# Performance work log

Hardware: AMD Instinct MI355X
Metric: run time of the kernel (lower is better)

Reference implementation:

```python
import jax, jax.numpy as jnp
import numpy as np

EMBED_DIM = 1024
NUM_HEADS = 16
HEAD_DIM = EMBED_DIM // NUM_HEADS
LN_EPS = 1e-5


def setup_inputs() -> dict:
    key = jax.random.key(0)
    ks = jax.random.split(key, 7)
    B, N, D = 4, 2048, EMBED_DIM
    s = 1.0 / np.sqrt(D)  # ~kaiming-uniform scale for Linear weights
    return {
        "inputs": jax.random.normal(ks[0], (B, N, D), dtype=jnp.float32),
        "W_q": jax.random.uniform(ks[1], (D, D), jnp.float32, -s, s),
        "W_k": jax.random.uniform(ks[2], (D, D), jnp.float32, -s, s),
        "W_v": jax.random.uniform(ks[3], (D, D), jnp.float32, -s, s),
        "W_o": jax.random.uniform(ks[4], (D, D), jnp.float32, -s, s),
        "ln_gamma": jnp.ones((D,), jnp.float32),
        "ln_beta": jnp.zeros((D,), jnp.float32),
    }


def reference(inputs, W_q, W_k, W_v, W_o, ln_gamma, ln_beta):
    x = inputs
    B, N, D = x.shape
    H, Hd = NUM_HEADS, HEAD_DIM
    # torch nn.Linear computes x @ W.T; W_* stored as (out, in)
    q = (x @ W_q.T).reshape(B, N, H, Hd).transpose(0, 2, 1, 3)  # [B,H,N,Hd]
    k = (x @ W_k.T).reshape(B, N, H, Hd).transpose(0, 2, 1, 3)
    v = (x @ W_v.T).reshape(B, N, H, Hd).transpose(0, 2, 1, 3)
    scores = jnp.einsum("bhqd,bhkd->bhqk", q, k) / jnp.sqrt(jnp.float32(Hd))
    attn = jax.nn.softmax(scores, axis=-1)  # dropout p=0 -> identity
    out = jnp.einsum("bhqk,bhkd->bhqd", attn, v)
    out = out.transpose(0, 2, 1, 3).reshape(B, N, D)
    out = out @ W_o.T
    # residual + LayerNorm
    y = out + x
    mu = jnp.mean(y, axis=-1, keepdims=True)
    var = jnp.mean(jnp.square(y - mu), axis=-1, keepdims=True)
    y = (y - mu) * jax.lax.rsqrt(var + LN_EPS)
    return y * ln_gamma + ln_beta
```

## Files before the change

### kernel.cpp

```cpp
#include <hip/hip_runtime.h>
#include <hip/hip_bf16.h>
#include <stdint.h>

typedef __attribute__((ext_vector_type(8))) short bf16x8;
typedef __attribute__((ext_vector_type(4))) float f32x4;

#define GLOBAL_AS __attribute__((address_space(1)))
#define LDS_AS    __attribute__((address_space(3)))

__device__ __forceinline__ void load_lds16(const void* g, void* l) {
  __builtin_amdgcn_global_load_lds((const GLOBAL_AS void*)g, (LDS_AS void*)l, 16, 0, 0);
}

__device__ __forceinline__ short f2bfn(float f) {
  __hip_bfloat16 h = __float2bfloat16(f);
  return __builtin_bit_cast(short, h);
}
__device__ __forceinline__ float bf2f(short s) {
  return __uint_as_float(((unsigned)(unsigned short)s) << 16);
}

__global__ __launch_bounds__(256) void cvt_all(const float* __restrict__ x,
                                               const float* __restrict__ q,
                                               const float* __restrict__ k,
                                               const float* __restrict__ v,
                                               const float* __restrict__ o,
                                               short* __restrict__ xb,
                                               short* __restrict__ Wb,
                                               short* __restrict__ Wob) {
  const int bid = blockIdx.x;
  const float* src;
  short* dst;
  int i;
  if (bid < 4096) {
    src = x; dst = xb; i = (bid * 256 + threadIdx.x) * 8;
  } else {
    const int sel = (bid - 4096) >> 9;
    const int inner = (bid - 4096) & 511;
    i = (inner * 256 + threadIdx.x) * 8;
    src = sel == 0 ? q : sel == 1 ? k : sel == 2 ? v : o;
    dst = sel == 0 ? Wb : sel == 1 ? Wb + 1024 * 1024
        : sel == 2 ? Wb + 2 * 1024 * 1024 : Wob;
  }
  float4 a = *(const float4*)(src + i);
  float4 b = *(const float4*)(src + i + 4);
  bf16x8 ov;
  ov[0] = f2bfn(a.x); ov[1] = f2bfn(a.y); ov[2] = f2bfn(a.z); ov[3] = f2bfn(a.w);
  ov[4] = f2bfn(b.x); ov[5] = f2bfn(b.y); ov[6] = f2bfn(b.z); ov[7] = f2bfn(b.w);
  *(bf16x8*)(dst + i) = ov;
}

__global__ __launch_bounds__(256) void gemm_qkvt(const short* __restrict__ xb,
                                                 const short* __restrict__ Wqk,
                                                 const short* __restrict__ Wv,
                                                 short* __restrict__ qkv,
                                                 short* __restrict__ VT) {
  __shared__ short As[128 * 64];
  __shared__ short Bs[128 * 64];
  const int t = threadIdx.x, l = t & 63, w = t >> 6;
  const int g = l >> 4, li = l & 15;
  const int wr = w >> 1, wc = w & 1;
  const int bid = blockIdx.x;
  const bool isqk = bid < 1024;
  const short* A;
  const short* B;
  int bm, bn;
  if (isqk) {
    A = xb; B = Wqk;
    bm = (bid & 7) * 8 + ((bid >> 3) & 7);
    bn = bid >> 6;
  } else {
    const int b2 = bid - 1024;
    A = Wv; B = xb;
    bm = b2 & 7;
    bn = b2 >> 3;
  }
  const int sw = li & 7;
  const int K = 1024;
  f32x4 acc[4][4] = {};
  const size_t arow0 = (size_t)(bm * 128) * K;
  const size_t brow0 = (size_t)(bn * 128) * K;
  for (int k0 = 0; k0 < K; k0 += 64) {
    __syncthreads();
#pragma unroll
    for (int it = 0; it < 4; ++it) {
      int e = it * 2048 + t * 8;
      int r = e >> 6;
      int cs = (e >> 3) & 7;
      int cg = cs ^ (r & 7);
      load_lds16(A + arow0 + (size_t)r * K + (k0 + cg * 8), &As[e]);
      load_lds16(B + brow0 + (size_t)r * K + (k0 + cg * 8), &Bs[e]);
    }
    __syncthreads();
#pragma unroll
    for (int kk = 0; kk < 2; ++kk) {
      bf16x8 af[4], bfr[4];
#pragma unroll
      for (int m = 0; m < 4; ++m)
        af[m] = *(const bf16x8*)&As[(wr * 64 + m * 16 + li) * 64 + (((kk * 4 + g) ^ sw) * 8)];
#pragma unroll
      for (int n = 0; n < 4; ++n)
        bfr[n] = *(const bf16x8*)&Bs[(wc * 64 + n * 16 + li) * 64 + (((kk * 4 + g) ^ sw) * 8)];
#pragma unroll
      for (int m = 0; m < 4; ++m)
#pragma unroll
        for (int n = 0; n < 4; ++n)
          acc[m][n] = __builtin_amdgcn_mfma_f32_16x16x32_bf16(af[m], bfr[n], acc[m][n], 0, 0, 0);
    }
  }
#pragma unroll
  for (int m = 0; m < 4; ++m)
#pragma unroll
    for (int n = 0; n < 4; ++n)
#pragma unroll
      for (int r = 0; r < 4; ++r) {
        int row = bm * 128 + wr * 64 + m * 16 + g * 4 + r;
        int col = bn * 128 + wc * 64 + n * 16 + li;
        if (isqk)
          qkv[(size_t)row * 3072 + col] = f2bfn(acc[m][n][r]);
        else
          VT[(size_t)(col >> 11) * (1024 * 2048) + (size_t)row * 2048 +
             (col & 2047)] = f2bfn(acc[m][n][r]);
      }
}

__global__ __launch_bounds__(256) void gemm_projres(const short* __restrict__ A,
                                                    const short* __restrict__ B,
                                                    const float* __restrict__ x,
                                                    short* __restrict__ Up) {
  __shared__ short As[128 * 64];
  __shared__ short Bs[128 * 64];
  const int t = threadIdx.x, l = t & 63, w = t >> 6;
  const int g = l >> 4, li = l & 15;
  const int wr = w >> 1, wc = w & 1;
  const int bid = blockIdx.x;
  const int bm = (bid & 7) * 8 + ((bid >> 3) & 7);
  const int bn = bid >> 6;
  const int sw = li & 7;
  const int K = 1024;
  f32x4 acc[4][4] = {};
  const size_t arow0 = (size_t)(bm * 128) * K;
  const size_t brow0 = (size_t)(bn * 128) * K;
  for (int k0 = 0; k0 < K; k0 += 64) {
    __syncthreads();
#pragma unroll
    for (int it = 0; it < 4; ++it) {
      int e = it * 2048 + t * 8;
      int r = e >> 6;
      int cs = (e >> 3) & 7;
      int cg = cs ^ (r & 7);
      load_lds16(A + arow0 + (size_t)r * K + (k0 + cg * 8), &As[e]);
      load_lds16(B + brow0 + (size_t)r * K + (k0 + cg * 8), &Bs[e]);
    }
    __syncthreads();
#pragma unroll
    for (int kk = 0; kk < 2; ++kk) {
      bf16x8 af[4], bfr[4];
#pragma unroll
      for (int m = 0; m < 4; ++m)
        af[m] = *(const bf16x8*)&As[(wr * 64 + m * 16 + li) * 64 + (((kk * 4 + g) ^ sw) * 8)];
#pragma unroll
      for (int n = 0; n < 4; ++n)
        bfr[n] = *(const bf16x8*)&Bs[(wc * 64 + n * 16 + li) * 64 + (((kk * 4 + g) ^ sw) * 8)];
#pragma unroll
      for (int m = 0; m < 4; ++m)
#pragma unroll
        for (int n = 0; n < 4; ++n)
          acc[m][n] = __builtin_amdgcn_mfma_f32_16x16x32_bf16(af[m], bfr[n], acc[m][n], 0, 0, 0);
    }
  }
#pragma unroll
  for (int m = 0; m < 4; ++m)
#pragma unroll
    for (int n = 0; n < 4; ++n)
#pragma unroll
      for (int r = 0; r < 4; ++r) {
        int row = bm * 128 + wr * 64 + m * 16 + g * 4 + r;
        int col = bn * 128 + wc * 64 + n * 16 + li;
        float v = acc[m][n][r] + x[(size_t)row * 1024 + col];
        Up[(size_t)row * 1024 + col] = f2bfn(v);
      }
}

__global__ __launch_bounds__(512, 4) void attn_fwd(const short* __restrict__ qkv,
                                                   const short* __restrict__ VT,
                                                   short* __restrict__ obuf) {
  const int f0 = blockIdx.x;
  const int work = (f0 & 7) * 64 + (f0 >> 3);
  const int qt = work & 7;
  const int bh = work >> 3;
  const int b = bh >> 4, h = bh & 15;
  const int t = threadIdx.x, w = t >> 6, l = t & 63;
  const int g = l >> 4, li = l & 15;

  __shared__ short Ks[2][64 * 64];
  __shared__ short Vts[2][64 * 64];
  __shared__ short Ps[8][2][16 * 64];

  const size_t base = (size_t)b * 2048 * 3072 + (size_t)h * 64;
  const short* Vsrc = VT + (size_t)bh * 64 * 2048;

  bf16x8 qf[2][2];
  {
    const float QSC = 0.125f * 1.44269504088896341f;
#pragma unroll
    for (int qh = 0; qh < 2; ++qh) {
      const short* qp = qkv + base + (size_t)(qt * 256 + w * 32 + qh * 16 + li) * 3072;
#pragma unroll
      for (int c = 0; c < 2; ++c) {
        bf16x8 v = *(const bf16x8*)(qp + c * 32 + g * 8);
#pragma unroll
        for (int i = 0; i < 8; ++i) {
          float f = bf2f(v[i]);
          v[i] = f2bfn(f * QSC);
        }
        qf[qh][c] = v;
      }
    }
  }

  bf16x8 ones;
#pragma unroll
  for (int i = 0; i < 8; ++i) ones[i] = (short)0x3F80;

  f32x4 o_[2][4], lacc[2];
#pragma unroll
  for (int qh = 0; qh < 2; ++qh) {
#pragma unroll
    for (int dj = 0; dj < 4; ++dj) o_[qh][dj] = (f32x4){0.f, 0.f, 0.f, 0.f};
    lacc[qh] = (f32x4){0.f, 0.f, 0.f, 0.f};
  }

  const int sw = li & 7;

#define STAGE(buf, kt_)                                                          \
  {                                                                              \
    int e = t * 8;                                                               \
    int r = e >> 6;                                                              \
    int cs = (e >> 3) & 7;                                                       \
    int cg = cs ^ (r & 7);                                                       \
    load_lds16(qkv + base + 1024 + (size_t)((kt_) * 64 + r) * 3072 + cg * 8,     \
               &Ks[buf][e]);                                                     \
    load_lds16(Vsrc + (size_t)r * 2048 + (kt_) * 64 + cg * 8, &Vts[buf][e]);     \
  }

  STAGE(0, 0);
  asm volatile("s_waitcnt vmcnt(0)" ::: "memory");
  __syncthreads();

  for (int kt = 0; kt < 32; ++kt) {
    const int cur = kt & 1;
    if (kt + 1 < 32) STAGE(cur ^ 1, kt + 1);

    f32x4 s_[2][4];
#pragma unroll
    for (int qh = 0; qh < 2; ++qh)
#pragma unroll
      for (int j = 0; j < 4; ++j) s_[qh][j] = (f32x4){0.f, 0.f, 0.f, 0.f};
    __builtin_amdgcn_s_setprio(1);
#pragma unroll
    for (int c = 0; c < 2; ++c)
#pragma unroll
      for (int j = 0; j < 4; ++j) {
        bf16x8 kf = *(const bf16x8*)&Ks[cur][(j * 16 + li) * 64 + (((c * 4 + g) ^ sw) * 8)];
        s_[0][j] = __builtin_amdgcn_mfma_f32_16x16x32_bf16(kf, qf[0][c], s_[0][j], 0, 0, 0);
        s_[1][j] = __builtin_amdgcn_mfma_f32_16x16x32_bf16(kf, qf[1][c], s_[1][j], 0, 0, 0);
      }
    __builtin_amdgcn_s_setprio(0);

#pragma unroll
    for (int qh = 0; qh < 2; ++qh) {
#pragma unroll
      for (int j = 0; j < 4; ++j) {
        float p0 = exp2f(s_[qh][j][0]);
        float p1 = exp2f(s_[qh][j][1]);
        float p2 = exp2f(s_[qh][j][2]);
        float p3 = exp2f(s_[qh][j][3]);
        unsigned u0, u1;
        asm("v_cvt_pk_bf16_f32 %0, %1, %2" : "=v"(u0) : "v"(p0), "v"(p1));
        asm("v_cvt_pk_bf16_f32 %0, %1, %2" : "=v"(u1) : "v"(p2), "v"(p3));
        uint2 pk2; pk2.x = u0; pk2.y = u1;
        int pos = (j * 16 + g * 4) ^ (sw << 3);
        *(uint2*)&Ps[w][qh][li * 64 + pos] = pk2;
      }
    }
    asm volatile("s_waitcnt lgkmcnt(0)" ::: "memory");

    __builtin_amdgcn_s_setprio(1);
#pragma unroll
    for (int c = 0; c < 2; ++c) {
      bf16x8 vb[4];
#pragma unroll
      for (int dj = 0; dj < 4; ++dj)
        vb[dj] = *(const bf16x8*)&Vts[cur][(dj * 16 + li) * 64 + (((c * 4 + g) ^ sw) * 8)];
#pragma unroll
      for (int qh = 0; qh < 2; ++qh) {
        bf16x8 pa = *(const bf16x8*)&Ps[w][qh][li * 64 + (((c * 4 + g) ^ sw) * 8)];
        lacc[qh] = __builtin_amdgcn_mfma_f32_16x16x32_bf16(pa, ones, lacc[qh], 0, 0, 0);
#pragma unroll
        for (int dj = 0; dj < 4; ++dj)
          o_[qh][dj] = __builtin_amdgcn_mfma_f32_16x16x32_bf16(pa, vb[dj], o_[qh][dj], 0, 0, 0);
      }
    }
    __builtin_amdgcn_s_setprio(0);

    asm volatile("s_waitcnt vmcnt(0)" ::: "memory");
    __syncthreads();
  }

#pragma unroll
  for (int qh = 0; qh < 2; ++qh)
#pragma unroll
    for (int r = 0; r < 4; ++r) {
      float ilr = 1.f / lacc[qh][r];
      int row = b * 2048 + qt * 256 + w * 32 + qh * 16 + g * 4 + r;
#pragma unroll
      for (int dj = 0; dj < 4; ++dj) {
        int col = h * 64 + dj * 16 + li;
        obuf[(size_t)row * 1024 + col] = f2bfn(o_[qh][dj][r] * ilr);
      }
    }
#undef STAGE
}

__global__ __launch_bounds__(256) void resid_ln(const short* __restrict__ Up,
                                                const float* __restrict__ gamma,
                                                const float* __restrict__ beta,
                                                float* __restrict__ out) {
  const int row = blockIdx.x;
  const int t = threadIdx.x, w = t >> 6, l = t & 63;
  short4 uv = *(const short4*)(Up + (size_t)row * 1024 + t * 4);
  float y[4] = {bf2f(uv.x), bf2f(uv.y), bf2f(uv.z), bf2f(uv.w)};
  float s = (y[0] + y[1]) + (y[2] + y[3]);
#pragma unroll
  for (int d = 1; d < 64; d <<= 1) s += __shfl_xor(s, d);
  __shared__ float red[4];
  if (l == 0) red[w] = s;
  __syncthreads();
  s = red[0] + red[1] + red[2] + red[3];
  const float mu = s * (1.f / 1024.f);
  float vs = 0.f;
#pragma unroll
  for (int i = 0; i < 4; ++i) { float d0 = y[i] - mu; vs += d0 * d0; }
#pragma unroll
  for (int d = 1; d < 64; d <<= 1) vs += __shfl_xor(vs, d);
  __syncthreads();
  if (l == 0) red[w] = vs;
  __syncthreads();
  vs = red[0] + red[1] + red[2] + red[3];
  const float rstd = rsqrtf(vs * (1.f / 1024.f) + 1e-5f);
  const float4 gg = *(const float4*)(gamma + t * 4);
  const float4 bb = *(const float4*)(beta + t * 4);
  float4 oo;
  oo.x = (y[0] - mu) * rstd * gg.x + bb.x;
  oo.y = (y[1] - mu) * rstd * gg.y + bb.y;
  oo.z = (y[2] - mu) * rstd * gg.z + bb.z;
  oo.w = (y[3] - mu) * rstd * gg.w + bb.w;
  *(float4*)(out + (size_t)row * 1024 + t * 4) = oo;
}

extern "C" void kernel_launch(void* const* d_in, const int* in_sizes, int n_in,
                              void* d_out, int out_size, void* d_ws, size_t ws_size,
                              hipStream_t stream) {
  const float* x     = (const float*)d_in[0];
  const float* W_q   = (const float*)d_in[1];
  const float* W_k   = (const float*)d_in[2];
  const float* W_v   = (const float*)d_in[3];
  const float* W_o   = (const float*)d_in[4];
  const float* gamma = (const float*)d_in[5];
  const float* beta  = (const float*)d_in[6];
  float* out = (float*)d_out;

  char* ws = (char*)d_ws;
  short* xb   = (short*)ws;  ws += (size_t)8192 * 1024 * 2;
  short* Wb   = (short*)ws;  ws += (size_t)3072 * 1024 * 2;
  short* Wob  = (short*)ws;  ws += (size_t)1024 * 1024 * 2;
  short* qkv  = (short*)ws;  ws += (size_t)8192 * 3072 * 2;
  short* obuf = (short*)ws;  ws += (size_t)8192 * 1024 * 2;
  short* Up   = (short*)ws;  ws += (size_t)8192 * 1024 * 2;
  short* VT   = (short*)ws;  ws += (size_t)64 * 64 * 2048 * 2;

  cvt_all<<<6144, 256, 0, stream>>>(x, W_q, W_k, W_v, W_o, xb, Wb, Wob);
  gemm_qkvt<<<1536, 256, 0, stream>>>(xb, Wb, Wb + 2 * 1024 * 1024, qkv, VT);
  attn_fwd<<<512, 512, 0, stream>>>(qkv, VT, obuf);
  gemm_projres<<<512, 256, 0, stream>>>(obuf, Wob, x, Up);
  resid_ln<<<8192, 256, 0, stream>>>(Up, gamma, beta, out);
}
```

Baseline: 215.8 us.

## Split QKV GEMM into double-buffered 256x256 QK kernel and separate VT kernel

The Q/K projection moves to a new kernel with 256x256 tiles, 512 threads, double-buffered LDS staging via async global-to-LDS loads, partial vmcnt waits and raised MFMA priority. This is meant to raise data reuse per tile and overlap loads with compute. The V-transpose GEMM becomes its own launch. The projection epilogue now reads the residual from the bf16 copy of x instead of fp32, which halves that read traffic but lowers residual precision.

```diff
diff --git a/kernel.cpp b/kernel.cpp
--- a/kernel.cpp
+++ b/kernel.cpp
@@ -50,31 +50,107 @@
   *(bf16x8*)(dst + i) = ov;
 }
 
-__global__ __launch_bounds__(256) void gemm_qkvt(const short* __restrict__ xb,
-                                                 const short* __restrict__ Wqk,
-                                                 const short* __restrict__ Wv,
-                                                 short* __restrict__ qkv,
-                                                 short* __restrict__ VT) {
+__global__ __launch_bounds__(512, 2) void gemm8_qk(const short* __restrict__ xb,
+                                                   const short* __restrict__ Wqk,
+                                                   short* __restrict__ qkv) {
+  __shared__ short As[2][256 * 64];
+  __shared__ short Bs[2][256 * 64];
+  const int t = threadIdx.x, l = t & 63, w = t >> 6;
+  const int g = l >> 4, li = l & 15, sw = li & 7;
+  const int wm = w >> 2, wn = w & 3;
+  const int bid = blockIdx.x;
+  const int work = (bid & 7) * 32 + (bid >> 3);
+  const int bm = work >> 3, bn = work & 7;
+  const int K = 1024;
+  const size_t arow0 = (size_t)(bm * 256) * K;
+  const size_t brow0 = (size_t)(bn * 256) * K;
+  f32x4 acc[8][4] = {};
+
+#define STAGE8(buf, k0_)                                                        \
+  {                                                                             \
+    _Pragma("unroll")                                                           \
+    for (int it = 0; it < 4; ++it) {                                            \
+      int e = it * 4096 + t * 8;                                                \
+      int r = e >> 6;                                                           \
+      int cg = (t & 7) ^ (r & 7);                                               \
+      load_lds16(xb + arow0 + (size_t)r * K + ((k0_) + cg * 8), &As[buf][e]);   \
+      load_lds16(Wqk + brow0 + (size_t)r * K + ((k0_) + cg * 8), &Bs[buf][e]);  \
+    }                                                                           \
+  }
+
+  STAGE8(0, 0);
+  for (int kt = 0; kt < 16; ++kt) {
+    const int cur = kt & 1;
+    if (kt < 15) {
+      STAGE8(cur ^ 1, (kt + 1) * 64);
+      asm volatile("s_waitcnt vmcnt(8)" ::: "memory");
+    } else {
+      asm volatile("s_waitcnt vmcnt(0)" ::: "memory");
+    }
+    __syncthreads();
+
+    bf16x8 afc[4][2];
+    bf16x8 bfc[4][2];
+#pragma unroll
+    for (int ph = 0; ph < 4; ++ph) {
+      const int mh = ph >> 1, nh = ph & 1;
+      if (nh == 0) {
+#pragma unroll
+        for (int m = 0; m < 4; ++m)
+#pragma unroll
+          for (int kk = 0; kk < 2; ++kk)
+            afc[m][kk] = *(const bf16x8*)&As[cur][(wm * 128 + (mh * 4 + m) * 16 + li) * 64 +
+                                                 (((kk * 4 + g) ^ sw) * 8)];
+      }
+      if (ph < 2) {
+#pragma unroll
+        for (int n2 = 0; n2 < 2; ++n2)
+#pragma unroll
+          for (int kk = 0; kk < 2; ++kk)
+            bfc[ph * 2 + n2][kk] = *(const bf16x8*)&Bs[cur][(wn * 64 + (ph * 2 + n2) * 16 + li) * 64 +
+                                                           (((kk * 4 + g) ^ sw) * 8)];
+      }
+      __syncthreads();
+      __builtin_amdgcn_s_setprio(1);
+#pragma unroll
+      for (int m = 0; m < 4; ++m)
+#pragma unroll
+        for (int n2 = 0; n2 < 2; ++n2)
+#pragma unroll
+          for (int kk = 0; kk < 2; ++kk) {
+            const int mi = mh * 4 + m, ni = nh * 2 + n2;
+            acc[mi][ni] = __builtin_amdgcn_mfma_f32_16x16x32_bf16(afc[m][kk], bfc[ni][kk],
+                                                                  acc[mi][ni], 0, 0, 0);
+          }
+      __builtin_amdgcn_s_setprio(0);
+      __syncthreads();
+    }
+  }
+#undef STAGE8
+
+#pragma unroll
+  for (int m = 0; m < 8; ++m)
+#pragma unroll
+    for (int n = 0; n < 4; ++n)
+#pragma unroll
+      for (int r = 0; r < 4; ++r) {
+        int row = bm * 256 + wm * 128 + m * 16 + g * 4 + r;
+        int col = bn * 256 + wn * 64 + n * 16 + li;
+        qkv[(size_t)row * 3072 + col] = f2bfn(acc[m][n][r]);
+      }
+}
+
+__global__ __launch_bounds__(256) void gemm_vt(const short* __restrict__ Wv,
+                                               const short* __restrict__ xb,
+                                               short* __restrict__ VT) {
   __shared__ short As[128 * 64];
   __shared__ short Bs[128 * 64];
   const int t = threadIdx.x, l = t & 63, w = t >> 6;
   const int g = l >> 4, li = l & 15;
   const int wr = w >> 1, wc = w & 1;
   const int bid = blockIdx.x;
-  const bool isqk = bid < 1024;
-  const short* A;
-  const short* B;
-  int bm, bn;
-  if (isqk) {
-    A = xb; B = Wqk;
-    bm = (bid & 7) * 8 + ((bid >> 3) & 7);
-    bn = bid >> 6;
-  } else {
-    const int b2 = bid - 1024;
-    A = Wv; B = xb;
-    bm = b2 & 7;
-    bn = b2 >> 3;
-  }
+  const int bm = bid & 7;
+  const int bn = bid >> 3;
   const int sw = li & 7;
   const int K = 1024;
   f32x4 acc[4][4] = {};
@@ -88,8 +164,8 @@
       int r = e >> 6;
       int cs = (e >> 3) & 7;
       int cg = cs ^ (r & 7);
-      load_lds16(A + arow0 + (size_t)r * K + (k0 + cg * 8), &As[e]);
-      load_lds16(B + brow0 + (size_t)r * K + (k0 + cg * 8), &Bs[e]);
+      load_lds16(Wv + arow0 + (size_t)r * K + (k0 + cg * 8), &As[e]);
+      load_lds16(xb + brow0 + (size_t)r * K + (k0 + cg * 8), &Bs[e]);
     }
     __syncthreads();
 #pragma unroll
@@ -116,17 +192,14 @@
       for (int r = 0; r < 4; ++r) {
         int row = bm * 128 + wr * 64 + m * 16 + g * 4 + r;
         int col = bn * 128 + wc * 64 + n * 16 + li;
-        if (isqk)
-          qkv[(size_t)row * 3072 + col] = f2bfn(acc[m][n][r]);
-        else
-          VT[(size_t)(col >> 11) * (1024 * 2048) + (size_t)row * 2048 +
-             (col & 2047)] = f2bfn(acc[m][n][r]);
+        VT[(size_t)(col >> 11) * (1024 * 2048) + (size_t)row * 2048 +
+           (col & 2047)] = f2bfn(acc[m][n][r]);
       }
 }
 
 __global__ __launch_bounds__(256) void gemm_projres(const short* __restrict__ A,
                                                     const short* __restrict__ B,
-                                                    const float* __restrict__ x,
+                                                    const short* __restrict__ xb,
                                                     short* __restrict__ Up) {
   __shared__ short As[128 * 64];
   __shared__ short Bs[128 * 64];
@@ -177,7 +250,7 @@
       for (int r = 0; r < 4; ++r) {
         int row = bm * 128 + wr * 64 + m * 16 + g * 4 + r;
         int col = bn * 128 + wc * 64 + n * 16 + li;
-        float v = acc[m][n][r] + x[(size_t)row * 1024 + col];
+        float v = acc[m][n][r] + bf2f(xb[(size_t)row * 1024 + col]);
         Up[(size_t)row * 1024 + col] = f2bfn(v);
       }
 }
@@ -381,8 +454,9 @@
   short* VT   = (short*)ws;  ws += (size_t)64 * 64 * 2048 * 2;
 
   cvt_all<<<6144, 256, 0, stream>>>(x, W_q, W_k, W_v, W_o, xb, Wb, Wob);
-  gemm_qkvt<<<1536, 256, 0, stream>>>(xb, Wb, Wb + 2 * 1024 * 1024, qkv, VT);
+  gemm8_qk<<<256, 512, 0, stream>>>(xb, Wb, qkv);
+  gemm_vt<<<512, 256, 0, stream>>>(Wb + 2 * 1024 * 1024, xb, VT);
   attn_fwd<<<512, 512, 0, stream>>>(qkv, VT, obuf);
-  gemm_projres<<<512, 256, 0, stream>>>(obuf, Wob, x, Up);
+  gemm_projres<<<512, 256, 0, stream>>>(obuf, Wob, xb, Up);
   resid_ln<<<8192, 256, 0, stream>>>(Up, gamma, beta, out);
 }
```

Result: no change. 214.9 us (-0.4%).
